# Kernel tuning notes

Measured on AMD Instinct MI355X. Metric: run time of the kernel, lower is better.

The kernel has to match this reference:

```python
import jax, jax.numpy as jnp
import numpy as np

DIM = 1024
NUM_HEADS = 16
HEAD_DIM = DIM // NUM_HEADS


def setup_inputs() -> dict:
    key = jax.random.key(0)
    k1, k2, k3, k4, k5 = jax.random.split(key, 5)
    B, N, C = 4, 4096, DIM
    s = 1.0 / np.sqrt(C)
    return {
        "x": jax.random.normal(k1, (B, N, C), dtype=jnp.float32),
        "W_qkv": jax.random.uniform(k2, (C, 3 * C), dtype=jnp.float32, minval=-s, maxval=s),
        "b_qkv": jax.random.uniform(k3, (3 * C,), dtype=jnp.float32, minval=-s, maxval=s),
        "W_proj": jax.random.uniform(k4, (C, C), dtype=jnp.float32, minval=-s, maxval=s),
        "b_proj": jax.random.uniform(k5, (C,), dtype=jnp.float32, minval=-s, maxval=s),
    }


def reference(x, W_qkv, b_qkv, W_proj, b_proj):
    B, N, C = x.shape
    H, D = NUM_HEADS, HEAD_DIM
    qkv = x @ W_qkv + b_qkv                      # [B,N,3C]
    qkv = qkv.reshape(B, N, 3, H, D).transpose(2, 0, 3, 1, 4)  # [3,B,H,N,D]
    q, k, v = qkv[0], qkv[1], qkv[2]
    q = jax.nn.softmax(q, axis=-1)               # softmax over head_dim
    k = jax.nn.softmax(k, axis=-2)               # softmax over sequence N
    context = jnp.einsum('bhnd,bhne->bhde', k, v)  # [B,H,D,D]
    out = jnp.einsum('bhnd,bhde->bhne', q, context)  # [B,H,N,D]
    out = out.transpose(0, 2, 1, 3).reshape(B, N, C)
    return out @ W_proj + b_proj
```

## Files before the change

### kernel.cpp

```cpp
#include <hip/hip_runtime.h>

#define BBATCH 4
#define SEQ 4096
#define CC 1024
#define HH 16
#define DD 64
#define TOKENS 16384
#define QKV3 3072

typedef __attribute__((ext_vector_type(8))) short short8;
typedef __attribute__((ext_vector_type(4))) float floatx4;

__device__ __forceinline__ unsigned short f2bf(float x) {
    unsigned int u = __float_as_uint(x);
    u += 0x7fff + ((u >> 16) & 1);
    return (unsigned short)(u >> 16);
}
__device__ __forceinline__ float bf2f(unsigned short h) {
    return __uint_as_float((unsigned int)h << 16);
}

__device__ __forceinline__ void gload_lds16(const void* g, void* l) {
    __builtin_amdgcn_global_load_lds(
        (const __attribute__((address_space(1))) unsigned int*)g,
        (__attribute__((address_space(3))) unsigned int*)l, 16, 0, 0);
}

__global__ __launch_bounds__(256) void cvt_bf16_kernel(
    const float* __restrict__ X, unsigned short* __restrict__ Y, long n4)
{
    long i = (long)blockIdx.x * 256 + threadIdx.x;
    if (i >= n4) return;
    float4 v = *reinterpret_cast<const float4*>(&X[i * 4]);
    ushort4 h;
    h.x = f2bf(v.x); h.y = f2bf(v.y); h.z = f2bf(v.z); h.w = f2bf(v.w);
    *reinterpret_cast<ushort4*>(&Y[i * 4]) = h;
}

__global__ __launch_bounds__(256) void transpose_bf16_kernel(
    const float* __restrict__ W, int K, int N, unsigned short* __restrict__ T)
{
    __shared__ unsigned short Lh[32][36];
    const int k0 = blockIdx.y * 32, n0 = blockIdx.x * 32;
    const int t = threadIdx.x;
    const int r = t >> 3, c4 = (t & 7) * 4;

    float4 w = *reinterpret_cast<const float4*>(&W[(size_t)(k0 + r) * N + n0 + c4]);
    Lh[r][c4 + 0] = f2bf(w.x);
    Lh[r][c4 + 1] = f2bf(w.y);
    Lh[r][c4 + 2] = f2bf(w.z);
    Lh[r][c4 + 3] = f2bf(w.w);
    __syncthreads();

    const int rn = t >> 3, ck = (t & 7) * 4;
    ushort4 h4;
    h4.x = Lh[ck + 0][rn]; h4.y = Lh[ck + 1][rn];
    h4.z = Lh[ck + 2][rn]; h4.w = Lh[ck + 3][rn];
    *reinterpret_cast<ushort4*>(&T[(size_t)(n0 + rn) * K + k0 + ck]) = h4;
}

template <int MODE>
__global__ __launch_bounds__(512) void gemm256_bf16_kernel(
    const unsigned short* __restrict__ A, int lda,
    const unsigned short* __restrict__ Bt, int ldb,
    const float* __restrict__ bias,
    float* __restrict__ Cf, int ldc,
    unsigned short* __restrict__ Qo, unsigned short* __restrict__ Ko,
    unsigned short* __restrict__ Vo)
{
    __shared__ unsigned short smem[65536];

    const int t = threadIdx.x;
    const int wave = t >> 6, lane = t & 63;

    const int gx = gridDim.x;
    const int nwg = gx * gridDim.y;
    const int id0 = blockIdx.y * gx + blockIdx.x;
    const int cpx = nwg >> 3;
    const int swzid = (id0 & 7) * cpx + (id0 >> 3);
    const int bx = swzid % gx, by = swzid / gx;

    const int row0 = by * 256, col0 = bx * 256;
    const int wave_m = wave >> 2, wave_n = wave & 3;

    const unsigned short* Bp = Bt;
    if (MODE == 0) Bp += ((size_t)(row0 >> 12)) << 20;

    const int fr  = lane & 15;
    const int fqb = (lane >> 4) << 4;
    const int sm  = (fr & 7) << 4;
    const int ck0 = ((0  + fqb) ^ sm) >> 1;
    const int ck1 = ((64 + fqb) ^ sm) >> 1;
    const int aRow = (wave_m * 128 + fr) * 64;
    const int bRow = (wave_n * 64 + fr) * 64;

    int srow[2], scol[2];
#pragma unroll
    for (int e = 0; e < 2; e++) {
        const int P  = (wave << 10) + (lane << 4) + (e << 13);
        const int r  = P >> 7;
        const int pc = P & 127;
        srow[e] = r;
        scol[e] = (pc ^ ((r & 7) << 4)) >> 1;
    }

    auto STAGE_PART = [&](int kt, int buf, int part) {
        const int isB = part >> 1, half = part & 1;
        const unsigned short* p = isB ? Bp : A;
        const int r0 = isB ? col0 : row0;
        const int ld = isB ? ldb : lda;
        const int ldsOff = buf * 32768 + isB * 16384 + half * 8192 + wave * 512;
#pragma unroll
        for (int e = 0; e < 2; e++)
            gload_lds16(&p[(size_t)(r0 + half * 128 + srow[e]) * ld
                           + ((kt & 15) << 6) + scol[e]],
                        &smem[ldsOff + e * 4096]);
    };

    floatx4 acc[8][4];
#pragma unroll
    for (int i = 0; i < 8; i++)
#pragma unroll
        for (int j = 0; j < 4; j++) acc[i][j] = (floatx4)0.0f;

    short8 a[4][2], bl[2][2], bh[2][2];

#define RDA(BUF, IH)                                                          \
    _Pragma("unroll") for (int ii = 0; ii < 4; ii++) {                        \
        a[ii][0] = *reinterpret_cast<const short8*>(                          \
            &smem[(BUF) * 32768 + aRow + ((IH) * 64 + ii * 16) * 64 + ck0]);  \
        a[ii][1] = *reinterpret_cast<const short8*>(                          \
            &smem[(BUF) * 32768 + aRow + ((IH) * 64 + ii * 16) * 64 + ck1]);  \
    }
#define RDB(BUF, JH, DST)                                                     \
    _Pragma("unroll") for (int jj = 0; jj < 2; jj++) {                        \
        DST[jj][0] = *reinterpret_cast<const short8*>(                        \
            &smem[(BUF) * 32768 + 16384 + bRow + ((JH) * 32 + jj * 16) * 64 + ck0]); \
        DST[jj][1] = *reinterpret_cast<const short8*>(                        \
            &smem[(BUF) * 32768 + 16384 + bRow + ((JH) * 32 + jj * 16) * 64 + ck1]); \
    }
#define MFMA_Q(IH, JH, BB)                                                    \
    __builtin_amdgcn_s_setprio(1);                                            \
    _Pragma("unroll") for (int ii = 0; ii < 4; ii++)                          \
    _Pragma("unroll") for (int jj = 0; jj < 2; jj++) {                        \
        acc[(IH)*4+ii][(JH)*2+jj] = __builtin_amdgcn_mfma_f32_16x16x32_bf16(  \
            a[ii][0], BB[jj][0], acc[(IH)*4+ii][(JH)*2+jj], 0, 0, 0);         \
        acc[(IH)*4+ii][(JH)*2+jj] = __builtin_amdgcn_mfma_f32_16x16x32_bf16(  \
            a[ii][1], BB[jj][1], acc[(IH)*4+ii][(JH)*2+jj], 0, 0, 0);         \
    }                                                                         \
    __builtin_amdgcn_s_setprio(0);
#define BARRIER __builtin_amdgcn_s_barrier()
#define WAIT_LGKM asm volatile("s_waitcnt lgkmcnt(0)" ::: "memory")
#define WAIT_VM2  asm volatile("s_waitcnt vmcnt(2)" ::: "memory")

#define KTILE(CUR, OTH, TN, TX)                                               \
    {                                                                         \
        RDA(CUR, 0); RDB(CUR, 0, bl);                                         \
        STAGE_PART(TN, OTH, 1);                                               \
        BARRIER; WAIT_LGKM; MFMA_Q(0, 0, bl); BARRIER;                        \
        RDB(CUR, 1, bh);                                                      \
        STAGE_PART(TN, OTH, 2);                                               \
        BARRIER; WAIT_LGKM; MFMA_Q(0, 1, bh); BARRIER;                        \
        RDA(CUR, 1);                                                          \
        STAGE_PART(TN, OTH, 3);                                               \
        BARRIER; WAIT_LGKM; MFMA_Q(1, 1, bh); BARRIER;                        \
        STAGE_PART(TX, CUR, 0);                                               \
        WAIT_VM2;                                                             \
        BARRIER;                                                              \
        MFMA_Q(1, 0, bl);                                                     \
        BARRIER;                                                              \
    }

    STAGE_PART(0, 0, 0); STAGE_PART(0, 0, 1);
    STAGE_PART(0, 0, 2); STAGE_PART(0, 0, 3);
    STAGE_PART(1, 1, 0);
    WAIT_VM2;
    BARRIER;

#pragma unroll 1
    for (int it = 0; it < 8; it++) {
        const int t1 = 2 * it + 1, t2 = 2 * it + 2, t3 = 2 * it + 3;
        KTILE(0, 1, t1, t2);
        KTILE(1, 0, t2, t3);
    }

#undef KTILE
#undef WAIT_VM2
#undef WAIT_LGKM
#undef BARRIER
#undef MFMA_Q
#undef RDB
#undef RDA

    const int cn = lane & 15, cq = (lane >> 4) * 4;
    if (MODE == 0) {
#pragma unroll
        for (int j = 0; j < 4; j++) {
            const int col = col0 + wave_n * 64 + j * 16 + cn;
            const float bv = bias[col];
#pragma unroll
            for (int i = 0; i < 8; i++)
#pragma unroll
                for (int r = 0; r < 4; r++) {
                    const int row = row0 + wave_m * 128 + i * 16 + cq + r;
                    Cf[(size_t)row * ldc + col] = acc[i][j][r] + bv;
                }
        }
    } else {
        unsigned short* outp = (bx < 4) ? Qo : ((bx < 8) ? Ko : Vo);
        const int f0 = col0 & 1023;
#pragma unroll
        for (int j = 0; j < 4; j++) {
            const int colg = col0 + wave_n * 64 + j * 16 + cn;
            const int f = f0 + wave_n * 64 + j * 16 + cn;
            const float bv = bias[colg];
#pragma unroll
            for (int i = 0; i < 8; i++)
#pragma unroll
                for (int r = 0; r < 4; r++) {
                    const int row = row0 + wave_m * 128 + i * 16 + cq + r;
                    outp[(size_t)row * CC + f] = f2bf(acc[i][j][r] + bv);
                }
        }
    }
}

__global__ __launch_bounds__(256) void q_softmax_kernel(unsigned short* __restrict__ Q)
{
    const int t = threadIdx.x;
    const long row = (long)blockIdx.x * 16 + (t >> 4);
    const int d4 = (t & 15) * 4;
    ushort4 hv = *reinterpret_cast<const ushort4*>(&Q[row * 64 + d4]);
    float v0 = bf2f(hv.x), v1 = bf2f(hv.y), v2 = bf2f(hv.z), v3 = bf2f(hv.w);
    float m = fmaxf(fmaxf(v0, v1), fmaxf(v2, v3));
#pragma unroll
    for (int s = 8; s > 0; s >>= 1) m = fmaxf(m, __shfl_xor(m, s));
    float e0 = __expf(v0 - m), e1 = __expf(v1 - m), e2 = __expf(v2 - m), e3 = __expf(v3 - m);
    float sum = e0 + e1 + e2 + e3;
#pragma unroll
    for (int s = 8; s > 0; s >>= 1) sum += __shfl_xor(sum, s);
    const float inv = 1.0f / sum;
    ushort4 o;
    o.x = f2bf(e0 * inv); o.y = f2bf(e1 * inv); o.z = f2bf(e2 * inv); o.w = f2bf(e3 * inv);
    *reinterpret_cast<ushort4*>(&Q[row * 64 + d4]) = o;
}

__global__ __launch_bounds__(256) void kv_ctx_kernel(
    const unsigned short* __restrict__ Km, const unsigned short* __restrict__ Vm,
    float* __restrict__ ctx, float* __restrict__ csum)
{
    const int bh = blockIdx.x, ch = blockIdx.y;
    const int b = bh >> 4, h = bh & 15;
    const int t = threadIdx.x;

    __shared__ float Ks[32][68];
    __shared__ float Vs[32][68];
    __shared__ float cred[4][64];

    const int d0 = (t >> 4) * 4, e0 = (t & 15) * 4;
    float acc[4][4];
#pragma unroll
    for (int i = 0; i < 4; i++)
#pragma unroll
        for (int j = 0; j < 4; j++) acc[i][j] = 0.0f;
    float csacc = 0.0f;
    const int dc = t & 63, rq = (t >> 6) * 8;

    const size_t base = (size_t)(b * SEQ + ch * 256) * CC + (size_t)h * 64;

    for (int n0 = 0; n0 < 256; n0 += 32) {
        __syncthreads();
#pragma unroll
        for (int l = 0; l < 2; l++) {
            const int idx = t + l * 256;
            const int r = idx >> 4, c4 = (idx & 15) * 4;
            ushort4 kv = *reinterpret_cast<const ushort4*>(&Km[base + (size_t)(n0 + r) * CC + c4]);
            ushort4 vv = *reinterpret_cast<const ushort4*>(&Vm[base + (size_t)(n0 + r) * CC + c4]);
            float4 kf;
            kf.x = __expf(bf2f(kv.x));
            kf.y = __expf(bf2f(kv.y));
            kf.z = __expf(bf2f(kv.z));
            kf.w = __expf(bf2f(kv.w));
            float4 vf = {bf2f(vv.x), bf2f(vv.y), bf2f(vv.z), bf2f(vv.w)};
            *reinterpret_cast<float4*>(&Ks[r][c4]) = kf;
            *reinterpret_cast<float4*>(&Vs[r][c4]) = vf;
        }
        __syncthreads();

#pragma unroll
        for (int r = 0; r < 8; r++) csacc += Ks[rq + r][dc];

#pragma unroll 8
        for (int n = 0; n < 32; n++) {
            float4 a = *reinterpret_cast<const float4*>(&Ks[n][d0]);
            float4 v4 = *reinterpret_cast<const float4*>(&Vs[n][e0]);
            float a4[4] = {a.x, a.y, a.z, a.w};
            float b4[4] = {v4.x, v4.y, v4.z, v4.w};
#pragma unroll
            for (int i = 0; i < 4; i++)
#pragma unroll
                for (int j = 0; j < 4; j++)
                    acc[i][j] += a4[i] * b4[j];
        }
    }

    __syncthreads();
    cred[t >> 6][dc] = csacc;
    __syncthreads();
    if (t < 64)
        atomicAdd(&csum[(size_t)bh * 64 + t],
                  cred[0][t] + cred[1][t] + cred[2][t] + cred[3][t]);

#pragma unroll
    for (int i = 0; i < 4; i++)
#pragma unroll
        for (int j = 0; j < 4; j++)
            atomicAdd(&ctx[((size_t)bh * 64 + d0 + i) * 64 + e0 + j], acc[i][j]);
}

__global__ __launch_bounds__(256) void weff_kernel(
    const float* __restrict__ ctx, const float* __restrict__ csum,
    const float* __restrict__ Wp, unsigned short* __restrict__ WeffT)
{
    const int bh = blockIdx.x, nc = blockIdx.y;
    const int b = bh >> 4, h = bh & 15;
    const int t = threadIdx.x;

    __shared__ float ctxs[64 * 64];
    __shared__ float cinvs[64];
#pragma unroll
    for (int l = 0; l < 16; l++)
        ctxs[t + l * 256] = ctx[(size_t)bh * 4096 + t + l * 256];
    if (t < 64) cinvs[t] = 1.0f / csum[(size_t)bh * 64 + t];
    __syncthreads();

    const int n = nc * 128 + (t & 127);
    const int dg = (t >> 7) * 32;

    float acc[32];
#pragma unroll
    for (int d = 0; d < 32; d++) acc[d] = 0.0f;

    for (int e = 0; e < 64; e++) {
        const float w = Wp[(size_t)(h * 64 + e) * CC + n];
#pragma unroll
        for (int d = 0; d < 32; d++)
            acc[d] += ctxs[(dg + d) * 64 + e] * w;
    }

    const size_t obase = ((size_t)b << 20) + (size_t)n * CC + h * 64 + dg;
#pragma unroll
    for (int d = 0; d < 32; d += 2) {
        ushort2 o;
        o.x = f2bf(acc[d] * cinvs[dg + d]);
        o.y = f2bf(acc[d + 1] * cinvs[dg + d + 1]);
        *reinterpret_cast<ushort2*>(&WeffT[obase + d]) = o;
    }
}

extern "C" void kernel_launch(void* const* d_in, const int* in_sizes, int n_in,
                              void* d_out, int out_size, void* d_ws, size_t ws_size,
                              hipStream_t stream)
{
    const float* x      = (const float*)d_in[0];
    const float* W_qkv  = (const float*)d_in[1];
    const float* b_qkv  = (const float*)d_in[2];
    const float* W_proj = (const float*)d_in[3];
    const float* b_proj = (const float*)d_in[4];
    float* out = (float*)d_out;

    unsigned short* Qm  = (unsigned short*)d_ws;
    unsigned short* Km  = Qm + (size_t)TOKENS * CC;
    unsigned short* Vm  = Km + (size_t)TOKENS * CC;
    unsigned short* xb  = Vm + (size_t)TOKENS * CC;
    unsigned short* wqT = xb + (size_t)TOKENS * CC;
    unsigned short* WeffT = wqT + (size_t)QKV3 * CC;
    float* ctx  = (float*)(WeffT + (size_t)BBATCH * CC * CC);
    float* csum = ctx + (size_t)64 * 64 * 64;

    hipMemsetAsync(ctx, 0, ((size_t)64 * 64 * 64 + 64 * 64) * sizeof(float), stream);

    cvt_bf16_kernel<<<(TOKENS * CC / 4 + 255) / 256, 256, 0, stream>>>(
        x, xb, (long)TOKENS * CC / 4);
    transpose_bf16_kernel<<<dim3(QKV3 / 32, CC / 32), 256, 0, stream>>>(
        W_qkv, CC, QKV3, wqT);

    gemm256_bf16_kernel<1><<<dim3(QKV3 / 256, TOKENS / 256), 512, 0, stream>>>(
        xb, CC, wqT, CC, b_qkv, (float*)nullptr, 0, Qm, Km, Vm);

    q_softmax_kernel<<<(TOKENS * HH) / 16, 256, 0, stream>>>(Qm);

    kv_ctx_kernel<<<dim3(BBATCH * HH, 16), 256, 0, stream>>>(Km, Vm, ctx, csum);

    weff_kernel<<<dim3(BBATCH * HH, 8), 256, 0, stream>>>(ctx, csum, W_proj, WeffT);

    gemm256_bf16_kernel<0><<<dim3(CC / 256, TOKENS / 256), 512, 0, stream>>>(
        Qm, CC, WeffT, CC, b_proj, out, CC, nullptr, nullptr, nullptr);
}
```

Baseline: 415.7 us.

## Fuse Q softmax into QKV GEMM epilogue and restage K-loop prefetch

The separate q_softmax kernel is removed; the MODE 1 GEMM epilogue now writes bias-added bf16 tiles to swizzled LDS, and each thread reads back 64-element head rows, applies softmax for Q blocks and stores with vectorized 16-byte writes. This drops a full read/write pass over Q and a launch, and makes the K/V stores coalesced as well. The K-loop staging is also reorganized to prefetch a whole tile two steps ahead, waiting with vmcnt(8) instead of vmcnt(2). In exchange the epilogue holds 64 floats per thread, which raises register pressure, and it adds two block-wide barriers.

```diff
diff --git a/kernel.cpp b/kernel.cpp
--- a/kernel.cpp
+++ b/kernel.cpp
@@ -151,21 +151,19 @@
     __builtin_amdgcn_s_setprio(0);
 #define BARRIER __builtin_amdgcn_s_barrier()
 #define WAIT_LGKM asm volatile("s_waitcnt lgkmcnt(0)" ::: "memory")
-#define WAIT_VM2  asm volatile("s_waitcnt vmcnt(2)" ::: "memory")
-
-#define KTILE(CUR, OTH, TN, TX)                                               \
+#define WAIT_VM8  asm volatile("s_waitcnt vmcnt(8)" ::: "memory")
+
+#define KTILE(CUR, TS)                                                        \
     {                                                                         \
         RDA(CUR, 0); RDB(CUR, 0, bl);                                         \
-        STAGE_PART(TN, OTH, 1);                                               \
         BARRIER; WAIT_LGKM; MFMA_Q(0, 0, bl); BARRIER;                        \
         RDB(CUR, 1, bh);                                                      \
-        STAGE_PART(TN, OTH, 2);                                               \
         BARRIER; WAIT_LGKM; MFMA_Q(0, 1, bh); BARRIER;                        \
         RDA(CUR, 1);                                                          \
-        STAGE_PART(TN, OTH, 3);                                               \
+        STAGE_PART(TS, CUR, 2); STAGE_PART(TS, CUR, 3);                       \
         BARRIER; WAIT_LGKM; MFMA_Q(1, 1, bh); BARRIER;                        \
-        STAGE_PART(TX, CUR, 0);                                               \
-        WAIT_VM2;                                                             \
+        STAGE_PART(TS, CUR, 0); STAGE_PART(TS, CUR, 1);                       \
+        WAIT_VM8;                                                             \
         BARRIER;                                                              \
         MFMA_Q(1, 0, bl);                                                     \
         BARRIER;                                                              \
@@ -173,19 +171,19 @@
 
     STAGE_PART(0, 0, 0); STAGE_PART(0, 0, 1);
     STAGE_PART(0, 0, 2); STAGE_PART(0, 0, 3);
-    STAGE_PART(1, 1, 0);
-    WAIT_VM2;
+    STAGE_PART(1, 1, 0); STAGE_PART(1, 1, 1);
+    STAGE_PART(1, 1, 2); STAGE_PART(1, 1, 3);
+    WAIT_VM8;
     BARRIER;
 
 #pragma unroll 1
     for (int it = 0; it < 8; it++) {
-        const int t1 = 2 * it + 1, t2 = 2 * it + 2, t3 = 2 * it + 3;
-        KTILE(0, 1, t1, t2);
-        KTILE(1, 0, t2, t3);
+        KTILE(0, (2 * it + 2) & 15);
+        KTILE(1, (2 * it + 3) & 15);
     }
 
 #undef KTILE
-#undef WAIT_VM2
+#undef WAIT_VM8
 #undef WAIT_LGKM
 #undef BARRIER
 #undef MFMA_Q
@@ -193,6 +191,7 @@
 #undef RDA
 
     const int cn = lane & 15, cq = (lane >> 4) * 4;
+
     if (MODE == 0) {
 #pragma unroll
         for (int j = 0; j < 4; j++) {
@@ -206,43 +205,70 @@
                     Cf[(size_t)row * ldc + col] = acc[i][j][r] + bv;
                 }
         }
-    } else {
+        return;
+    }
+
+    __syncthreads();
+
+#pragma unroll
+    for (int j = 0; j < 4; j++) {
+        const int colL = wave_n * 64 + j * 16 + cn;
+        const float bv = bias[col0 + colL];
+#pragma unroll
+        for (int i = 0; i < 8; i++)
+#pragma unroll
+            for (int r = 0; r < 4; r++) {
+                const int lr = wave_m * 128 + i * 16 + cq + r;
+                smem[lr * 256 + (colL ^ ((lr & 7) << 3))] = f2bf(acc[i][j][r] + bv);
+            }
+    }
+    __syncthreads();
+
+    {
         unsigned short* outp = (bx < 4) ? Qo : ((bx < 8) ? Ko : Vo);
-        const int f0 = col0 & 1023;
-#pragma unroll
-        for (int j = 0; j < 4; j++) {
-            const int colg = col0 + wave_n * 64 + j * 16 + cn;
-            const int f = f0 + wave_n * 64 + j * 16 + cn;
-            const float bv = bias[colg];
-#pragma unroll
-            for (int i = 0; i < 8; i++)
-#pragma unroll
-                for (int r = 0; r < 4; r++) {
-                    const int row = row0 + wave_m * 128 + i * 16 + cq + r;
-                    outp[(size_t)row * CC + f] = f2bf(acc[i][j][r] + bv);
+        const bool isQ = (bx < 4);
+        const int R = t >> 1, half = t & 1;
+        const size_t obase = (size_t)(row0 + R) * CC + (col0 & 1023) + half * 128;
+        unsigned short* orow = &outp[obase];
+
+#pragma unroll
+        for (int g = 0; g < 2; g++) {
+            short8 bufv[8];
+            const int cbase = half * 16 + g * 8;
+#pragma unroll
+            for (int k = 0; k < 8; k++)
+                bufv[k] = *reinterpret_cast<const short8*>(
+                    &smem[R * 256 + (((cbase + k) ^ (R & 7)) << 3)]);
+            if (isQ) {
+                float v[64];
+                float mx = -3.0e38f;
+#pragma unroll
+                for (int k = 0; k < 8; k++)
+#pragma unroll
+                    for (int e = 0; e < 8; e++) {
+                        const float f = bf2f((unsigned short)bufv[k][e]);
+                        v[k * 8 + e] = f;
+                        mx = fmaxf(mx, f);
+                    }
+                float s = 0.0f;
+#pragma unroll
+                for (int q = 0; q < 64; q++) {
+                    const float ev = __expf(v[q] - mx);
+                    v[q] = ev;
+                    s += ev;
                 }
+                const float inv = 1.0f / s;
+#pragma unroll
+                for (int k = 0; k < 8; k++)
+#pragma unroll
+                    for (int e = 0; e < 8; e++)
+                        bufv[k][e] = (short)f2bf(v[k * 8 + e] * inv);
+            }
+#pragma unroll
+            for (int k = 0; k < 8; k++)
+                *reinterpret_cast<short8*>(&orow[g * 64 + k * 8]) = bufv[k];
         }
     }
-}
-
-__global__ __launch_bounds__(256) void q_softmax_kernel(unsigned short* __restrict__ Q)
-{
-    const int t = threadIdx.x;
-    const long row = (long)blockIdx.x * 16 + (t >> 4);
-    const int d4 = (t & 15) * 4;
-    ushort4 hv = *reinterpret_cast<const ushort4*>(&Q[row * 64 + d4]);
-    float v0 = bf2f(hv.x), v1 = bf2f(hv.y), v2 = bf2f(hv.z), v3 = bf2f(hv.w);
-    float m = fmaxf(fmaxf(v0, v1), fmaxf(v2, v3));
-#pragma unroll
-    for (int s = 8; s > 0; s >>= 1) m = fmaxf(m, __shfl_xor(m, s));
-    float e0 = __expf(v0 - m), e1 = __expf(v1 - m), e2 = __expf(v2 - m), e3 = __expf(v3 - m);
-    float sum = e0 + e1 + e2 + e3;
-#pragma unroll
-    for (int s = 8; s > 0; s >>= 1) sum += __shfl_xor(sum, s);
-    const float inv = 1.0f / sum;
-    ushort4 o;
-    o.x = f2bf(e0 * inv); o.y = f2bf(e1 * inv); o.z = f2bf(e2 * inv); o.w = f2bf(e3 * inv);
-    *reinterpret_cast<ushort4*>(&Q[row * 64 + d4]) = o;
 }
 
 __global__ __launch_bounds__(256) void kv_ctx_kernel(
@@ -388,8 +414,6 @@
     gemm256_bf16_kernel<1><<<dim3(QKV3 / 256, TOKENS / 256), 512, 0, stream>>>(
         xb, CC, wqT, CC, b_qkv, (float*)nullptr, 0, Qm, Km, Vm);
 
-    q_softmax_kernel<<<(TOKENS * HH) / 16, 256, 0, stream>>>(Qm);
-
     kv_ctx_kernel<<<dim3(BBATCH * HH, 16), 256, 0, stream>>>(Km, Vm, ctx, csum);
 
     weff_kernel<<<dim3(BBATCH * HH, 8), 256, 0, stream>>>(ctx, csum, W_proj, WeffT);
```

Result: no change. 413.2 us (-0.6%).
